# Performance work log

Hardware: AMD Instinct MI355X
Metric: run time of the kernel (lower is better)

## Reference

```python
import jax, jax.numpy as jnp
import numpy as np

EPS = 1e-05
RMS_EPS = 1e-06


def activation_quant(x, num_bits=8):
    # per-token (last-dim) abs-max int8 fake quant, computed in fp32
    qn = -(2 ** (num_bits - 1))
    qp = 2 ** (num_bits - 1) - 1
    xf = x.astype(jnp.float32)
    s = qp / jnp.clip(jnp.max(jnp.abs(xf), axis=-1, keepdims=True), EPS, None)
    return (jnp.clip(jnp.round(xf * s), qn, qp) / s).astype(x.dtype)


def weight_quant(w):
    # full-tensor abs-mean ternary fake quant
    wf = w.astype(jnp.float32)
    s = 1.0 / jnp.clip(jnp.mean(jnp.abs(wf)), EPS, None)
    return (jnp.clip(jnp.round(wf * s), -1.0, 1.0) / s).astype(w.dtype)


def bit_linear(x, w):
    # STE wrappers (identity in forward value, straight-through in grad)
    qx = x + jax.lax.stop_gradient(activation_quant(x) - x)
    qw = w + jax.lax.stop_gradient(weight_quant(w) - w)
    return jnp.einsum('bsh,oh->bso', qx, qw)


def rms_norm(x, weight, eps=RMS_EPS):
    xf = x.astype(jnp.float32)
    var = jnp.mean(xf * xf, axis=-1, keepdims=True)
    return weight * (xf * jax.lax.rsqrt(var + eps)).astype(x.dtype)


def setup_inputs() -> dict:
    key = jax.random.key(0)
    k1, k2, k3, k4 = jax.random.split(key, 4)
    B, S, H, I = 2, 2048, 2048, 8192
    scale = 1.0 / np.sqrt(H)
    return {
        'x': jax.random.normal(k1, (B, S, H), dtype=jnp.float32),
        'w_gate': jax.random.normal(k2, (I, H), dtype=jnp.float32) * scale,
        'w_up': jax.random.normal(k3, (I, H), dtype=jnp.float32) * scale,
        'w_down': jax.random.normal(k4, (H, I), dtype=jnp.float32) * (1.0 / np.sqrt(I)),
        'ln_weight': jnp.ones((I,), dtype=jnp.float32),
    }


def reference(x, w_gate, w_up, w_down, ln_weight):
    h = jax.nn.silu(bit_linear(x, w_gate)) * bit_linear(x, w_up)
    h = rms_norm(h, ln_weight)
    return bit_linear(h, w_down)
```

## Files before the change

kernel.cpp:

```cpp
#include <hip/hip_runtime.h>
#include <stdint.h>

typedef int v4i __attribute__((ext_vector_type(4)));

#define TOKENS 4096
#define HDIM   2048
#define IDIM   8192
#define WN     16777216
#define NBLK   512
#define BANDP  5e-7f

#define MFMA_I8 __builtin_amdgcn_mfma_i32_16x16x64_i8

static __device__ __forceinline__ void gload_lds16(const void* g, void* l) {
  __builtin_amdgcn_global_load_lds(
      (const __attribute__((address_space(1))) void*)(unsigned long long)(uintptr_t)g,
      (__attribute__((address_space(3))) void*)(unsigned)(uintptr_t)l,
      16, 0, 0);
}

static __device__ __forceinline__ double wsum64d(double v) {
#pragma unroll
  for (int m = 32; m; m >>= 1) v += __shfl_xor(v, m, 64);
  return v;
}
static __device__ __forceinline__ double wmax64d(double v) {
#pragma unroll
  for (int m = 32; m; m >>= 1) v = fmax(v, __shfl_xor(v, m, 64));
  return v;
}
static __device__ __forceinline__ float wmax64f(float v) {
#pragma unroll
  for (int m = 32; m; m >>= 1) v = fmaxf(v, __shfl_xor(v, m, 64));
  return v;
}

static __device__ __forceinline__ int q8f(float v, float s, float lo, float hi) {
  float p = v * s;
  return (int)fminf(fmaxf(rintf(p), lo), hi);
}
static __device__ __forceinline__ uint32_t packq_f(float4 v, float s) {
  int a = q8f(v.x, s, -128.f, 127.f);
  int b = q8f(v.y, s, -128.f, 127.f);
  int c = q8f(v.z, s, -128.f, 127.f);
  int d = q8f(v.w, s, -128.f, 127.f);
  return (uint32_t)((a & 255) | ((b & 255) << 8) | ((c & 255) << 16) | ((d & 255) << 24));
}

__global__ __launch_bounds__(256) void wsum_leaf(const float* __restrict__ wg,
                                                 const float* __restrict__ wu,
                                                 const float* __restrict__ wd,
                                                 float* __restrict__ part) {
  const float* w = blockIdx.y == 0 ? wg : (blockIdx.y == 1 ? wu : wd);
  int tid = threadIdx.x;
  const float4* w4 = (const float4*)w;
  size_t base4 = ((size_t)blockIdx.x * 256 + tid) * 32;
  float4 p = w4[base4], q = w4[base4 + 1];
  float r0 = fabsf(p.x), r1 = fabsf(p.y), r2 = fabsf(p.z), r3 = fabsf(p.w);
  float r4 = fabsf(q.x), r5 = fabsf(q.y), r6 = fabsf(q.z), r7 = fabsf(q.w);
  for (int i = 2; i < 32; i += 2) {
    float4 a = w4[base4 + i], b = w4[base4 + i + 1];
    r0 += fabsf(a.x); r1 += fabsf(a.y); r2 += fabsf(a.z); r3 += fabsf(a.w);
    r4 += fabsf(b.x); r5 += fabsf(b.y); r6 += fabsf(b.z); r7 += fabsf(b.w);
  }
  float leaf = ((r0 + r1) + (r2 + r3)) + ((r4 + r5) + (r6 + r7));
  __shared__ float A[256], B[256];
  A[tid] = leaf;
  __syncthreads();
  float* src = A; float* dst = B;
  for (int n = 128; n >= 1; n >>= 1) {
    if (tid < n) dst[tid] = src[2 * tid] + src[2 * tid + 1];
    __syncthreads();
    float* t = src; src = dst; dst = t;
  }
  if (tid == 0) part[blockIdx.y * NBLK + blockIdx.x] = src[0];
}

__global__ __launch_bounds__(256) void wsum_final(const float* __restrict__ part,
                                                  float* __restrict__ wsc) {
  int t = blockIdx.x, tid = threadIdx.x;
  __shared__ float A[512], B[256];
  A[tid] = part[t * NBLK + tid];
  A[tid + 256] = part[t * NBLK + tid + 256];
  __syncthreads();
  float* src = A; float* dst = B;
  for (int n = 256; n >= 1; n >>= 1) {
    if (tid < n) dst[tid] = src[2 * tid] + src[2 * tid + 1];
    __syncthreads();
    float* tmp = src; src = dst; dst = tmp;
  }
  if (tid == 0) {
    float mean32 = src[0] / (float)WN;
    float m32 = fmaxf(mean32, 1e-5f);
    float s32 = 1.0f / m32;
    wsc[t] = s32;
    wsc[3 + t] = 1.0f / s32;
  }
}

__global__ __launch_bounds__(256) void wquant_kernel(const float* __restrict__ wg,
                                                     const float* __restrict__ wu,
                                                     const float* __restrict__ wd,
                                                     const float* __restrict__ wsc,
                                                     int8_t* __restrict__ qg,
                                                     int8_t* __restrict__ qu,
                                                     int8_t* __restrict__ qd) {
  int t = blockIdx.y;
  const float* w = t == 0 ? wg : (t == 1 ? wu : wd);
  int8_t* q = t == 0 ? qg : (t == 1 ? qu : qd);
  float s32 = wsc[t];
  const float4* w4 = (const float4*)w;
  uint32_t* q4 = (uint32_t*)q;
  const int n4 = WN / 4;
  for (int i = blockIdx.x * 256 + threadIdx.x; i < n4; i += gridDim.x * 256) {
    float4 v = w4[i];
    float vv[4] = {v.x, v.y, v.z, v.w};
    int o[4];
#pragma unroll
    for (int j = 0; j < 4; ++j) {
      float pf = fabsf(vv[j]) * s32;
      int q2 = 2 * (int)fminf(rintf(pf), 1.0f);
      if (fabsf(pf - 0.5f) < BANDP) q2 = 1;
      o[j] = (vv[j] < 0.0f) ? -q2 : q2;
    }
    q4[i] = (uint32_t)((o[0] & 255) | ((o[1] & 255) << 8) |
                       ((o[2] & 255) << 16) | ((o[3] & 255) << 24));
  }
}

__global__ __launch_bounds__(256) void xquant_kernel(const float* __restrict__ x,
                                                     int8_t* __restrict__ qx,
                                                     double* __restrict__ axd) {
  int row = blockIdx.x, tid = threadIdx.x;
  const float4* xr = (const float4*)(x + (size_t)row * HDIM);
  float4 v0 = xr[tid], v1 = xr[tid + 256];
  float m = fmaxf(fmaxf(fmaxf(fabsf(v0.x), fabsf(v0.y)), fmaxf(fabsf(v0.z), fabsf(v0.w))),
                  fmaxf(fmaxf(fabsf(v1.x), fabsf(v1.y)), fmaxf(fabsf(v1.z), fabsf(v1.w))));
  m = wmax64f(m);
  __shared__ float red[4];
  int wid = tid >> 6, lane = tid & 63;
  if (lane == 0) red[wid] = m;
  __syncthreads();
  float mm = fmaxf(fmaxf(red[0], red[1]), fmaxf(red[2], red[3]));
  float c32 = fmaxf(mm, 1e-5f);
  float s32 = 127.0f / c32;
  if (tid == 0) axd[row] = 1.0 / (double)s32;
  uint32_t* q4 = (uint32_t*)(qx + (size_t)row * HDIM);
  q4[tid] = packq_f(v0, s32);
  q4[tid + 256] = packq_f(v1, s32);
}

__global__ __launch_bounds__(512, 4) void gemm1_kernel(const int8_t* __restrict__ qx,
                                                       const int8_t* __restrict__ qg,
                                                       const int8_t* __restrict__ qu,
                                                       const float* __restrict__ wsc,
                                                       const double* __restrict__ axd,
                                                       float* __restrict__ h) {
  extern __shared__ char lds[];
  int tid = threadIdx.x, wid = tid >> 6, lane = tid & 63;
  int l15 = lane & 15, lgp = lane >> 4;
  int wr = wid >> 2, wc = wid & 3;
  int flat = blockIdx.y * 64 + blockIdx.x;
  int xcd = flat & 7, local = flat >> 3;
  int mt = local >> 3, nl = local & 7;
  int m0 = mt * 128, n0 = (xcd * 8 + nl) * 128;
  const int8_t* bA = qx + (size_t)m0 * HDIM;
  const int8_t* bG = qg + (size_t)n0 * HDIM;
  const int8_t* bU = qu + (size_t)n0 * HDIM;

  v4i accg[4][2], accu[4][2];
  v4i vzero = {0, 0, 0, 0};
#pragma unroll
  for (int i = 0; i < 4; ++i)
#pragma unroll
    for (int j = 0; j < 2; ++j) { accg[i][j] = vzero; accu[i][j] = vzero; }

  int aoff[4], goff[2], uoff[2];
#pragma unroll
  for (int i = 0; i < 4; ++i)
    aoff[i] = lgp * 2048 + (wr * 64 + i * 16 + l15) * 16;
#pragma unroll
  for (int i = 0; i < 2; ++i) {
    goff[i] = 8192 + lgp * 2048 + (wc * 32 + i * 16 + l15) * 16;
    uoff[i] = goff[i] + 8192;
  }

  int srow = tid & 127, sslab = tid >> 7;
  const size_t rA = (size_t)srow * HDIM;
  int sdst = sslab * 2048 + srow * 16;

  const int NT = HDIM / 64;
  {
    size_t k0 = (size_t)sslab * 16;
    gload_lds16(bA + rA + k0, lds + sdst);
    gload_lds16(bG + rA + k0, lds + sdst + 8192);
    gload_lds16(bU + rA + k0, lds + sdst + 16384);
    size_t k1 = 64 + (size_t)sslab * 16;
    gload_lds16(bA + rA + k1, lds + 24576 + sdst);
    gload_lds16(bG + rA + k1, lds + 24576 + sdst + 8192);
    gload_lds16(bU + rA + k1, lds + 24576 + sdst + 16384);
  }
  asm volatile("s_waitcnt vmcnt(3)" ::: "memory");
  __builtin_amdgcn_s_barrier();
  __builtin_amdgcn_sched_barrier(0);

  int c0 = 0, c1 = 24576, c2 = 49152;
  for (int t = 0; t < NT; ++t) {
    const bool pf = (t + 2 < NT);
    size_t koff = (size_t)(t + 2) * 64 + sslab * 16;
    v4i a0 = *(const v4i*)(lds + c0 + aoff[0]);
    v4i a1 = *(const v4i*)(lds + c0 + aoff[1]);
    v4i bg0 = *(const v4i*)(lds + c0 + goff[0]);
    v4i bg1 = *(const v4i*)(lds + c0 + goff[1]);
    if (pf) gload_lds16(bA + rA + koff, lds + c2 + sdst);
    __builtin_amdgcn_s_barrier();
    asm volatile("s_waitcnt lgkmcnt(0)" ::: "memory");
    __builtin_amdgcn_sched_barrier(0);
    __builtin_amdgcn_s_setprio(1);
    accg[0][0] = MFMA_I8(a0, bg0, accg[0][0], 0, 0, 0);
    accg[0][1] = MFMA_I8(a0, bg1, accg[0][1], 0, 0, 0);
    accg[1][0] = MFMA_I8(a1, bg0, accg[1][0], 0, 0, 0);
    accg[1][1] = MFMA_I8(a1, bg1, accg[1][1], 0, 0, 0);
    __builtin_amdgcn_s_setprio(0);
    __builtin_amdgcn_s_barrier();
    v4i a2 = *(const v4i*)(lds + c0 + aoff[2]);
    v4i a3 = *(const v4i*)(lds + c0 + aoff[3]);
    if (pf) gload_lds16(bG + rA + koff, lds + c2 + sdst + 8192);
    __builtin_amdgcn_s_barrier();
    asm volatile("s_waitcnt lgkmcnt(0)" ::: "memory");
    __builtin_amdgcn_sched_barrier(0);
    __builtin_amdgcn_s_setprio(1);
    accg[2][0] = MFMA_I8(a2, bg0, accg[2][0], 0, 0, 0);
    accg[2][1] = MFMA_I8(a2, bg1, accg[2][1], 0, 0, 0);
    accg[3][0] = MFMA_I8(a3, bg0, accg[3][0], 0, 0, 0);
    accg[3][1] = MFMA_I8(a3, bg1, accg[3][1], 0, 0, 0);
    __builtin_amdgcn_s_setprio(0);
    __builtin_amdgcn_s_barrier();
    v4i bu0 = *(const v4i*)(lds + c0 + uoff[0]);
    v4i bu1 = *(const v4i*)(lds + c0 + uoff[1]);
    if (pf) gload_lds16(bU + rA + koff, lds + c2 + sdst + 16384);
    __builtin_amdgcn_s_barrier();
    asm volatile("s_waitcnt lgkmcnt(0)" ::: "memory");
    __builtin_amdgcn_sched_barrier(0);
    __builtin_amdgcn_s_setprio(1);
    accu[0][0] = MFMA_I8(a0, bu0, accu[0][0], 0, 0, 0);
    accu[0][1] = MFMA_I8(a0, bu1, accu[0][1], 0, 0, 0);
    accu[1][0] = MFMA_I8(a1, bu0, accu[1][0], 0, 0, 0);
    accu[1][1] = MFMA_I8(a1, bu1, accu[1][1], 0, 0, 0);
    __builtin_amdgcn_s_setprio(0);
    __builtin_amdgcn_s_barrier();
    if (pf)
      asm volatile("s_waitcnt vmcnt(3)" ::: "memory");
    else
      asm volatile("s_waitcnt vmcnt(0)" ::: "memory");
    __builtin_amdgcn_s_barrier();
    __builtin_amdgcn_sched_barrier(0);
    __builtin_amdgcn_s_setprio(1);
    accu[2][0] = MFMA_I8(a2, bu0, accu[2][0], 0, 0, 0);
    accu[2][1] = MFMA_I8(a2, bu1, accu[2][1], 0, 0, 0);
    accu[3][0] = MFMA_I8(a3, bu0, accu[3][0], 0, 0, 0);
    accu[3][1] = MFMA_I8(a3, bu1, accu[3][1], 0, 0, 0);
    __builtin_amdgcn_s_setprio(0);
    __builtin_amdgcn_s_barrier();
    int tmp = c0; c0 = c1; c1 = c2; c2 = tmp;
  }

  double mg = 0.5 * (double)wsc[3 + 0];
  double mu = 0.5 * (double)wsc[3 + 1];
#pragma unroll
  for (int mi = 0; mi < 4; ++mi) {
#pragma unroll
    for (int rg = 0; rg < 4; ++rg) {
      int grow = m0 + wr * 64 + mi * 16 + lgp * 4 + rg;
      double axr = axd[grow];
      double sg = axr * mg, su = axr * mu;
#pragma unroll
      for (int ni = 0; ni < 2; ++ni) {
        int gcol = n0 + wc * 32 + ni * 16 + l15;
        double g = (double)accg[mi][ni][rg] * sg;
        double u = (double)accu[mi][ni][rg] * su;
        double sig = 1.0 / (1.0 + exp(-g));
        h[(size_t)grow * IDIM + gcol] = (float)((g * sig) * u);
      }
    }
  }
}

__global__ __launch_bounds__(256) void hquant_kernel(const float* __restrict__ h,
                                                     const float* __restrict__ lnw,
                                                     double* __restrict__ ahd,
                                                     int8_t* __restrict__ qh) {
  int row = blockIdx.x, tid = threadIdx.x;
  const float4* hr = (const float4*)(h + (size_t)row * IDIM);
  const float4* lw4 = (const float4*)lnw;
  float4 hv[8], wv[8];
  double ssq = 0.0;
#pragma unroll
  for (int i = 0; i < 8; ++i) {
    hv[i] = hr[tid + i * 256];
    wv[i] = lw4[tid + i * 256];
    ssq += (double)hv[i].x * hv[i].x + (double)hv[i].y * hv[i].y +
           (double)hv[i].z * hv[i].z + (double)hv[i].w * hv[i].w;
  }
  ssq = wsum64d(ssq);
  __shared__ double redd[4];
  __shared__ double redm[4];
  int wid = tid >> 6, lane = tid & 63;
  if (lane == 0) redd[wid] = ssq;
  __syncthreads();
  double tot = redd[0] + redd[1] + redd[2] + redd[3];
  double rd = 1.0 / sqrt(tot * (1.0 / (double)IDIM) + 1e-6);
  double mx = 0.0;
#pragma unroll
  for (int i = 0; i < 8; ++i) {
    double y0 = (double)wv[i].x * ((double)hv[i].x * rd);
    double y1 = (double)wv[i].y * ((double)hv[i].y * rd);
    double y2 = (double)wv[i].z * ((double)hv[i].z * rd);
    double y3 = (double)wv[i].w * ((double)hv[i].w * rd);
    mx = fmax(mx, fmax(fmax(fabs(y0), fabs(y1)), fmax(fabs(y2), fabs(y3))));
  }
  mx = wmax64d(mx);
  if (lane == 0) redm[wid] = mx;
  __syncthreads();
  double mm = fmax(fmax(redm[0], redm[1]), fmax(redm[2], redm[3]));
  float c32 = fmaxf((float)mm, 1e-5f);
  float s32 = 127.0f / c32;
  double sd = (double)s32;
  if (tid == 0) ahd[row] = 1.0 / (double)s32;
  uint32_t* q4 = (uint32_t*)(qh + (size_t)row * IDIM);
#pragma unroll
  for (int i = 0; i < 8; ++i) {
    double y0 = (double)wv[i].x * ((double)hv[i].x * rd);
    double y1 = (double)wv[i].y * ((double)hv[i].y * rd);
    double y2 = (double)wv[i].z * ((double)hv[i].z * rd);
    double y3 = (double)wv[i].w * ((double)hv[i].w * rd);
    int a = (int)fmin(fmax(rint(y0 * sd), -128.0), 127.0);
    int b = (int)fmin(fmax(rint(y1 * sd), -128.0), 127.0);
    int c = (int)fmin(fmax(rint(y2 * sd), -128.0), 127.0);
    int d = (int)fmin(fmax(rint(y3 * sd), -128.0), 127.0);
    q4[tid + i * 256] = (uint32_t)((a & 255) | ((b & 255) << 8) | ((c & 255) << 16) | ((d & 255) << 24));
  }
}

__global__ __launch_bounds__(512, 4) void gemm2_kernel(const int8_t* __restrict__ qh,
                                                       const int8_t* __restrict__ qd,
                                                       const float* __restrict__ wsc,
                                                       const double* __restrict__ ahd,
                                                       float* __restrict__ out) {
  extern __shared__ char lds[];
  int tid = threadIdx.x, wid = tid >> 6, lane = tid & 63;
  int l15 = lane & 15, lgp = lane >> 4;
  int wr = wid >> 2, wc = wid & 3;
  int flat = blockIdx.y * 16 + blockIdx.x;
  int xcd = flat & 7, local = flat >> 3;
  int mt = xcd * 4 + (local >> 4), nt = local & 15;
  int m0 = mt * 128, n0 = nt * 128;
  const int8_t* bA = qh + (size_t)m0 * IDIM;
  const int8_t* bB = qd + (size_t)n0 * IDIM;

  v4i acc[4][2];
  v4i vzero = {0, 0, 0, 0};
#pragma unroll
  for (int i = 0; i < 4; ++i)
#pragma unroll
    for (int j = 0; j < 2; ++j) acc[i][j] = vzero;

  int aoff[4], boff[2];
#pragma unroll
  for (int i = 0; i < 4; ++i)
    aoff[i] = lgp * 2048 + (wr * 64 + i * 16 + l15) * 16;
#pragma unroll
  for (int i = 0; i < 2; ++i)
    boff[i] = 8192 + lgp * 2048 + (wc * 32 + i * 16 + l15) * 16;

  int srow = tid & 127, sslab = tid >> 7;
  const size_t rA = (size_t)srow * IDIM;
  int sdst = sslab * 2048 + srow * 16;

  const int NT = IDIM / 64;
  {
    size_t k0 = (size_t)sslab * 16;
    gload_lds16(bA + rA + k0, lds + sdst);
    gload_lds16(bB + rA + k0, lds + sdst + 8192);
    size_t k1 = 64 + (size_t)sslab * 16;
    gload_lds16(bA + rA + k1, lds + 16384 + sdst);
    gload_lds16(bB + rA + k1, lds + 16384 + sdst + 8192);
  }
  asm volatile("s_waitcnt vmcnt(2)" ::: "memory");
  __builtin_amdgcn_s_barrier();
  __builtin_amdgcn_sched_barrier(0);

  int c0 = 0, c1 = 16384, c2 = 32768;
  for (int t = 0; t < NT; ++t) {
    const bool pf = (t + 2 < NT);
    size_t koff = (size_t)(t + 2) * 64 + sslab * 16;
    v4i a0 = *(const v4i*)(lds + c0 + aoff[0]);
    v4i a1 = *(const v4i*)(lds + c0 + aoff[1]);
    v4i b0 = *(const v4i*)(lds + c0 + boff[0]);
    v4i b1 = *(const v4i*)(lds + c0 + boff[1]);
    if (pf) gload_lds16(bA + rA + koff, lds + c2 + sdst);
    __builtin_amdgcn_s_barrier();
    asm volatile("s_waitcnt lgkmcnt(0)" ::: "memory");
    __builtin_amdgcn_sched_barrier(0);
    __builtin_amdgcn_s_setprio(1);
    acc[0][0] = MFMA_I8(a0, b0, acc[0][0], 0, 0, 0);
    acc[0][1] = MFMA_I8(a0, b1, acc[0][1], 0, 0, 0);
    acc[1][0] = MFMA_I8(a1, b0, acc[1][0], 0, 0, 0);
    acc[1][1] = MFMA_I8(a1, b1, acc[1][1], 0, 0, 0);
    __builtin_amdgcn_s_setprio(0);
    __builtin_amdgcn_s_barrier();
    v4i a2 = *(const v4i*)(lds + c0 + aoff[2]);
    v4i a3 = *(const v4i*)(lds + c0 + aoff[3]);
    if (pf) gload_lds16(bB + rA + koff, lds + c2 + sdst + 8192);
    if (pf)
      asm volatile("s_waitcnt vmcnt(2)" ::: "memory");
    else
      asm volatile("s_waitcnt vmcnt(0)" ::: "memory");
    __builtin_amdgcn_s_barrier();
    asm volatile("s_waitcnt lgkmcnt(0)" ::: "memory");
    __builtin_amdgcn_sched_barrier(0);
    __builtin_amdgcn_s_setprio(1);
    acc[2][0] = MFMA_I8(a2, b0, acc[2][0], 0, 0, 0);
    acc[2][1] = MFMA_I8(a2, b1, acc[2][1], 0, 0, 0);
    acc[3][0] = MFMA_I8(a3, b0, acc[3][0], 0, 0, 0);
    acc[3][1] = MFMA_I8(a3, b1, acc[3][1], 0, 0, 0);
    __builtin_amdgcn_s_setprio(0);
    __builtin_amdgcn_s_barrier();
    int tmp = c0; c0 = c1; c1 = c2; c2 = tmp;
  }

  double md = 0.5 * (double)wsc[3 + 2];
#pragma unroll
  for (int mi = 0; mi < 4; ++mi) {
#pragma unroll
    for (int rg = 0; rg < 4; ++rg) {
      int grow = m0 + wr * 64 + mi * 16 + lgp * 4 + rg;
      double sc = ahd[grow] * md;
#pragma unroll
      for (int ni = 0; ni < 2; ++ni) {
        int gcol = n0 + wc * 32 + ni * 16 + l15;
        out[(size_t)grow * HDIM + gcol] = (float)((double)acc[mi][ni][rg] * sc);
      }
    }
  }
}

extern "C" void kernel_launch(void* const* d_in, const int* in_sizes, int n_in,
                              void* d_out, int out_size, void* d_ws, size_t ws_size,
                              hipStream_t stream) {
  const float* x   = (const float*)d_in[0];
  const float* wg  = (const float*)d_in[1];
  const float* wu  = (const float*)d_in[2];
  const float* wd  = (const float*)d_in[3];
  const float* lnw = (const float*)d_in[4];
  float* out = (float*)d_out;
  char* ws = (char*)d_ws;

  size_t off = 0;
  auto alloc = [&](size_t b) { size_t o = off; off += (b + 255) & ~(size_t)255; return o; };
  size_t o_wsc  = alloc(8 * 4);
  size_t o_part = alloc(3 * NBLK * 4);
  size_t o_axd  = alloc((size_t)TOKENS * 8);
  size_t o_ahd  = alloc((size_t)TOKENS * 8);
  size_t o_qx   = alloc((size_t)TOKENS * HDIM);
  size_t o_qg   = alloc((size_t)IDIM * HDIM);
  size_t o_qu   = alloc((size_t)IDIM * HDIM);
  size_t o_qd   = alloc((size_t)HDIM * IDIM);
  size_t o_h    = alloc((size_t)TOKENS * IDIM * 4);
  (void)ws_size; (void)in_sizes; (void)n_in; (void)out_size; (void)o_qu;

  float* wsc  = (float*)(ws + o_wsc);
  float* part = (float*)(ws + o_part);
  double* axd = (double*)(ws + o_axd);
  double* ahd = (double*)(ws + o_ahd);
  int8_t* qx  = (int8_t*)(ws + o_qx);
  int8_t* qg  = (int8_t*)(ws + o_qg);
  int8_t* qu  = (int8_t*)(ws + o_qu);
  int8_t* qd  = (int8_t*)(ws + o_qd);
  int8_t* qh  = (int8_t*)(ws + o_qg);
  float* h    = (float*)(ws + o_h);

  wsum_leaf<<<dim3(NBLK, 3), 256, 0, stream>>>(wg, wu, wd, part);
  wsum_final<<<3, 256, 0, stream>>>(part, wsc);
  wquant_kernel<<<dim3(1024, 3), 256, 0, stream>>>(wg, wu, wd, wsc, qg, qu, qd);
  xquant_kernel<<<TOKENS, 256, 0, stream>>>(x, qx, axd);
  gemm1_kernel<<<dim3(IDIM / 128, TOKENS / 128), 512, 3 * 24576, stream>>>(qx, qg, qu, wsc, axd, h);
  hquant_kernel<<<TOKENS, 256, 0, stream>>>(h, lnw, ahd, qh);
  gemm2_kernel<<<dim3(HDIM / 128, TOKENS / 128), 512, 3 * 16384, stream>>>(qh, qd, wsc, ahd, out);
}
```

Before: 495.4 us.

## Merge gate/up GEMM phases into two stages and coalesce weight-sum leaf loads

The gate/up int8 MFMA main loop goes from four barrier-separated phases per k-step to two. All A fragments are loaded up front and two of the three prefetch loads are issued together, which cuts the number of s_barrier/waitcnt points per iteration. The vmcnt wait now happens before the up-phase barrier. The weight abs-sum leaf kernel is also restructured so each pair of adjacent lanes reads interleaved float4s of one leaf and combines them with a shuffle, which improves coalescing. Holding a2/a3 live across more of the loop raises register pressure, and there is less fine-grained interleaving of loads with MFMAs.

```diff
diff --git a/kernel.cpp b/kernel.cpp
--- a/kernel.cpp
+++ b/kernel.cpp
@@ -53,19 +53,24 @@
                                                  float* __restrict__ part) {
   const float* w = blockIdx.y == 0 ? wg : (blockIdx.y == 1 ? wu : wd);
   int tid = threadIdx.x;
+  int wv = tid >> 6, lane = tid & 63;
+  int lf = lane >> 1, m = lane & 1;
+  __shared__ float A[256], B[256];
   const float4* w4 = (const float4*)w;
-  size_t base4 = ((size_t)blockIdx.x * 256 + tid) * 32;
-  float4 p = w4[base4], q = w4[base4 + 1];
-  float r0 = fabsf(p.x), r1 = fabsf(p.y), r2 = fabsf(p.z), r3 = fabsf(p.w);
-  float r4 = fabsf(q.x), r5 = fabsf(q.y), r6 = fabsf(q.z), r7 = fabsf(q.w);
-  for (int i = 2; i < 32; i += 2) {
-    float4 a = w4[base4 + i], b = w4[base4 + i + 1];
-    r0 += fabsf(a.x); r1 += fabsf(a.y); r2 += fabsf(a.z); r3 += fabsf(a.w);
-    r4 += fabsf(b.x); r5 += fabsf(b.y); r6 += fabsf(b.z); r7 += fabsf(b.w);
-  }
-  float leaf = ((r0 + r1) + (r2 + r3)) + ((r4 + r5) + (r6 + r7));
-  __shared__ float A[256], B[256];
-  A[tid] = leaf;
+#pragma unroll
+  for (int p = 0; p < 2; ++p) {
+    int leaf = wv * 64 + p * 32 + lf;
+    size_t b4 = ((size_t)blockIdx.x * 256 + leaf) * 32;
+    float4 v = w4[b4 + m];
+    float r0 = fabsf(v.x), r1 = fabsf(v.y), r2 = fabsf(v.z), r3 = fabsf(v.w);
+    for (int k = 1; k < 16; ++k) {
+      float4 u = w4[b4 + m + 2 * k];
+      r0 += fabsf(u.x); r1 += fabsf(u.y); r2 += fabsf(u.z); r3 += fabsf(u.w);
+    }
+    float s = (r0 + r1) + (r2 + r3);
+    float o = __shfl_xor(s, 1, 64);
+    if (m == 0) A[leaf] = s + o;
+  }
   __syncthreads();
   float* src = A; float* dst = B;
   for (int n = 128; n >= 1; n >>= 1) {
@@ -210,9 +215,14 @@
     size_t koff = (size_t)(t + 2) * 64 + sslab * 16;
     v4i a0 = *(const v4i*)(lds + c0 + aoff[0]);
     v4i a1 = *(const v4i*)(lds + c0 + aoff[1]);
+    v4i a2 = *(const v4i*)(lds + c0 + aoff[2]);
+    v4i a3 = *(const v4i*)(lds + c0 + aoff[3]);
     v4i bg0 = *(const v4i*)(lds + c0 + goff[0]);
     v4i bg1 = *(const v4i*)(lds + c0 + goff[1]);
-    if (pf) gload_lds16(bA + rA + koff, lds + c2 + sdst);
+    if (pf) {
+      gload_lds16(bA + rA + koff, lds + c2 + sdst);
+      gload_lds16(bG + rA + koff, lds + c2 + sdst + 8192);
+    }
     __builtin_amdgcn_s_barrier();
     asm volatile("s_waitcnt lgkmcnt(0)" ::: "memory");
     __builtin_amdgcn_sched_barrier(0);
@@ -221,15 +231,6 @@
     accg[0][1] = MFMA_I8(a0, bg1, accg[0][1], 0, 0, 0);
     accg[1][0] = MFMA_I8(a1, bg0, accg[1][0], 0, 0, 0);
     accg[1][1] = MFMA_I8(a1, bg1, accg[1][1], 0, 0, 0);
-    __builtin_amdgcn_s_setprio(0);
-    __builtin_amdgcn_s_barrier();
-    v4i a2 = *(const v4i*)(lds + c0 + aoff[2]);
-    v4i a3 = *(const v4i*)(lds + c0 + aoff[3]);
-    if (pf) gload_lds16(bG + rA + koff, lds + c2 + sdst + 8192);
-    __builtin_amdgcn_s_barrier();
-    asm volatile("s_waitcnt lgkmcnt(0)" ::: "memory");
-    __builtin_amdgcn_sched_barrier(0);
-    __builtin_amdgcn_s_setprio(1);
     accg[2][0] = MFMA_I8(a2, bg0, accg[2][0], 0, 0, 0);
     accg[2][1] = MFMA_I8(a2, bg1, accg[2][1], 0, 0, 0);
     accg[3][0] = MFMA_I8(a3, bg0, accg[3][0], 0, 0, 0);
@@ -239,6 +240,10 @@
     v4i bu0 = *(const v4i*)(lds + c0 + uoff[0]);
     v4i bu1 = *(const v4i*)(lds + c0 + uoff[1]);
     if (pf) gload_lds16(bU + rA + koff, lds + c2 + sdst + 16384);
+    if (pf)
+      asm volatile("s_waitcnt vmcnt(3)" ::: "memory");
+    else
+      asm volatile("s_waitcnt vmcnt(0)" ::: "memory");
     __builtin_amdgcn_s_barrier();
     asm volatile("s_waitcnt lgkmcnt(0)" ::: "memory");
     __builtin_amdgcn_sched_barrier(0);
@@ -247,15 +252,6 @@
     accu[0][1] = MFMA_I8(a0, bu1, accu[0][1], 0, 0, 0);
     accu[1][0] = MFMA_I8(a1, bu0, accu[1][0], 0, 0, 0);
     accu[1][1] = MFMA_I8(a1, bu1, accu[1][1], 0, 0, 0);
-    __builtin_amdgcn_s_setprio(0);
-    __builtin_amdgcn_s_barrier();
-    if (pf)
-      asm volatile("s_waitcnt vmcnt(3)" ::: "memory");
-    else
-      asm volatile("s_waitcnt vmcnt(0)" ::: "memory");
-    __builtin_amdgcn_s_barrier();
-    __builtin_amdgcn_sched_barrier(0);
-    __builtin_amdgcn_s_setprio(1);
     accu[2][0] = MFMA_I8(a2, bu0, accu[2][0], 0, 0, 0);
     accu[2][1] = MFMA_I8(a2, bu1, accu[2][1], 0, 0, 0);
     accu[3][0] = MFMA_I8(a3, bu0, accu[3][0], 0, 0, 0);
```

After: 501.2 us. About the same (+1.2%).
